# Kernel tuning notes

Hardware: AMD Instinct MI355X
Metric: run time of the kernel (lower is better)

## Reference

```python
import jax, jax.numpy as jnp
import numpy as np

RES_IN, RES_OUT, STRIDE = 14, 7, 2
H1, KD1, AR1 = 4, 32, 2    # per-layer attention blocks
H2, KD2, AR2 = 8, 32, 4    # subsample attention block
DEPTHS = 4


def _bias_idxs(res):
    pts = [(i, j) for i in range(res) for j in range(res)]
    offs, idx = {}, []
    for p1 in pts:
        for p2 in pts:
            o = (abs(p1[0] - p2[0]), abs(p1[1] - p2[1]))
            if o not in offs:
                offs[o] = len(offs)
            idx.append(offs[o])
    return np.array(idx, np.int32).reshape(len(pts), len(pts)), len(offs)


def _bias_idxs_sub(res_in, res_out, stride):
    pts = [(i, j) for i in range(res_in) for j in range(res_in)]
    pts_ = [(i, j) for i in range(res_out) for j in range(res_out)]
    offs, idx = {}, []
    for p1 in pts_:
        for p2 in pts:
            o = (abs(p1[0] * stride - p2[0]), abs(p1[1] * stride - p2[1]))
            if o not in offs:
                offs[o] = len(offs)
            idx.append(offs[o])
    return np.array(idx, np.int32).reshape(len(pts_), len(pts)), len(offs)

IDX1, NOFF1 = _bias_idxs(RES_IN)                     # [196,196], 196 offsets
IDX2, NOFF2 = _bias_idxs_sub(RES_IN, RES_OUT, STRIDE)  # [49,196], 196 offsets


def hardswish(x):
    return x * jnp.clip(x + 3.0, 0.0, 6.0) * (1.0 / 6.0)


def setup_inputs() -> dict:
    key = jax.random.key(0)
    ks = iter(jax.random.split(key, 64))

    def nrm(shape, scale=1.0):
        return jax.random.normal(next(ks), shape, jnp.float32) * scale

    def lin(shape):  # fan-in scaled linear weight, last dim = in_features
        return nrm(shape, (1.0 / shape[-1]) ** 0.5)

    def bn(shape):  # folded BN (scale, shift)
        return 1.0 + nrm(shape, 0.05), nrm(shape, 0.05)

    B, S, C = 256, RES_IN * RES_IN, 256
    d = {"x": nrm((B, S, C))}
    d["attn_Wqkv"] = lin((DEPTHS, 512, 256))
    d["attn_qkv_s"], d["attn_qkv_t"] = bn((DEPTHS, 512))
    d["attn_Wproj"] = lin((DEPTHS, 256, 256))
    d["attn_proj_s"], d["attn_proj_t"] = bn((DEPTHS, 256))
    d["attn_bias"] = nrm((DEPTHS, H1, NOFF1), 0.02)
    d["mlp_W1"] = lin((DEPTHS, 512, 256))
    d["mlp1_s"], d["mlp1_t"] = bn((DEPTHS, 512))
    d["mlp_W2"] = lin((DEPTHS, 256, 512))
    d["mlp2_s"], d["mlp2_t"] = bn((DEPTHS, 256))
    d["sub_Wkv"] = lin((1280, 256))
    d["sub_kv_s"], d["sub_kv_t"] = bn((1280,))
    d["sub_Wq"] = lin((256, 256))
    d["sub_q_s"], d["sub_q_t"] = bn((256,))
    d["sub_Wproj"] = lin((384, 1024))
    d["sub_proj_s"], d["sub_proj_t"] = bn((384,))
    d["sub_bias"] = nrm((H2, NOFF2), 0.02)
    d["smlp_W1"] = lin((768, 384))
    d["smlp1_s"], d["smlp1_t"] = bn((768,))
    d["smlp_W2"] = lin((384, 768))
    d["smlp2_s"], d["smlp2_t"] = bn((384,))
    return d


def reference(x, attn_Wqkv, attn_qkv_s, attn_qkv_t, attn_Wproj, attn_proj_s,
              attn_proj_t, attn_bias, mlp_W1, mlp1_s, mlp1_t, mlp_W2, mlp2_s,
              mlp2_t, sub_Wkv, sub_kv_s, sub_kv_t, sub_Wq, sub_q_s, sub_q_t,
              sub_Wproj, sub_proj_s, sub_proj_t, sub_bias, smlp_W1, smlp1_s,
              smlp1_t, smlp_W2, smlp2_s, smlp2_t):
    B, S, C = x.shape
    idx1 = jnp.asarray(IDX1)
    idx2 = jnp.asarray(IDX2)
    scale1 = KD1 ** -0.5
    scale2 = KD2 ** -0.5

    # DEPTHS x (residual attention + residual MLP), eval-mode BN folded to scale/shift
    for l in range(DEPTHS):
        qkv = (x @ attn_Wqkv[l].T) * attn_qkv_s[l] + attn_qkv_t[l]      # [B,S,512]
        qkv = qkv.reshape(B, S, H1, 2 * KD1 + AR1 * KD1)
        q, k, v = qkv[..., :KD1], qkv[..., KD1:2 * KD1], qkv[..., 2 * KD1:]
        logits = jnp.einsum('bqhd,bkhd->bhqk', q, k) * scale1 + attn_bias[l][:, idx1]
        a = jax.nn.softmax(logits, axis=-1)
        o = jnp.einsum('bhqk,bkhd->bqhd', a, v).reshape(B, S, H1 * AR1 * KD1)
        x = x + ((hardswish(o) @ attn_Wproj[l].T) * attn_proj_s[l] + attn_proj_t[l])
        h = hardswish((x @ mlp_W1[l].T) * mlp1_s[l] + mlp1_t[l])
        x = x + ((h @ mlp_W2[l].T) * mlp2_s[l] + mlp2_t[l])

    # attention subsample block (no residual on attention path)
    kv = ((x @ sub_Wkv.T) * sub_kv_s + sub_kv_t).reshape(B, S, H2, KD2 + AR2 * KD2)
    k, v = kv[..., :KD2], kv[..., KD2:]
    xq = x.reshape(B, RES_IN, RES_IN, C)[:, ::STRIDE, ::STRIDE].reshape(B, RES_OUT * RES_OUT, C)
    q = ((xq @ sub_Wq.T) * sub_q_s + sub_q_t).reshape(B, RES_OUT * RES_OUT, H2, KD2)
    logits = jnp.einsum('bqhd,bkhd->bhqk', q, k) * scale2 + sub_bias[:, idx2]
    a = jax.nn.softmax(logits, axis=-1)
    o = jnp.einsum('bhqk,bkhd->bqhd', a, v).reshape(B, RES_OUT * RES_OUT, H2 * AR2 * KD2)
    x = (hardswish(o) @ sub_Wproj.T) * sub_proj_s + sub_proj_t            # [B,49,384]

    # residual MLP after subsample
    h = hardswish((x @ smlp_W1.T) * smlp1_s + smlp1_t)
    x = x + ((h @ smlp_W2.T) * smlp2_s + smlp2_t)
    return x
```

## Files before the change

kernel.cpp:

```cpp
#include <hip/hip_runtime.h>

typedef __attribute__((ext_vector_type(8))) short s16x8;
typedef __attribute__((ext_vector_type(4))) short s16x4;
typedef __attribute__((ext_vector_type(4))) float f32x4;
typedef __attribute__((ext_vector_type(8))) __fp16 f16x8;
typedef __attribute__((ext_vector_type(2))) __fp16 f16x2;

#define AS1 __attribute__((address_space(1)))
#define AS3 __attribute__((address_space(3)))

__device__ __forceinline__ short h16(float f) {
  __fp16 t = (__fp16)f;
  return *(short*)&t;
}
__device__ __forceinline__ float h2f(short s) {
  __fp16 t = *(__fp16*)&s;
  return (float)t;
}
__device__ __forceinline__ unsigned pkh2(float a, float b) {
  f16x2 h = __builtin_amdgcn_cvt_pkrtz(a, b);
  return *(unsigned*)&h;
}
__device__ __forceinline__ float hswish(float v) { return v * fminf(fmaxf(v + 3.f, 0.f), 6.f) * (1.f / 6.f); }
__device__ __forceinline__ int iabs(int v) { return v < 0 ? -v : v; }
__device__ __forceinline__ int gmap(int r) {
  int bb = r / 49, p = r - bb * 49;
  int i = p / 7, j = p - i * 7;
  return bb * 196 + i * 28 + j * 2;
}

template <int ACT, int RES, int WF, int WH, int GATHER>
__global__ __launch_bounds__(256) void gemm_k(
    const short* __restrict__ A, const short* __restrict__ W,
    const float* __restrict__ sc, const float* __restrict__ tc,
    const short* __restrict__ Rs, float* __restrict__ oF, short* __restrict__ oH,
    int M, int N, int K, int nwg) {
  __shared__ __align__(16) short As[128 * 64];
  __shared__ __align__(16) short Bs[128 * 64];
  const int tid = threadIdx.x;
  const int lane = tid & 63;
  const int wave = tid >> 6;
  const int wm = wave >> 1, wn = wave & 1;
  const int r15 = lane & 15, kq = lane >> 4;

  const int qc = nwg >> 3, rc = nwg & 7;
  const int xcd = blockIdx.x & 7, off = blockIdx.x >> 3;
  const int wg = (xcd < rc) ? xcd * (qc + 1) + off : rc * (qc + 1) + (xcd - rc) * qc + off;
  const int NTt = N >> 7;
  const int nt = wg % NTt, mt = wg / NTt;
  const int m0 = mt << 7, n0 = nt << 7;

  const int tr = tid >> 3;
  const int col8 = (tid & 7) ^ (tr & 7);
  const short* pa = A + (size_t)(m0 + tr) * K + 8 * col8;
  const short* pb = W + (size_t)(n0 + tr) * K + 8 * col8;
  short* la = As + tid * 8;
  short* lb = Bs + tid * 8;

  f32x4 acc[4][4] = {};
  const int NT = K >> 6;

#define ISSUE(kt)                                                                     \
  {                                                                                   \
    _Pragma("unroll") for (int i = 0; i < 4; ++i) {                                   \
      const short* ga;                                                                \
      if (GATHER)                                                                     \
        ga = A + (size_t)gmap(m0 + tr + 32 * i) * K + 8 * col8 + (kt) * 64;           \
      else                                                                            \
        ga = pa + (size_t)(32 * i) * K + (kt) * 64;                                   \
      __builtin_amdgcn_global_load_lds((const AS1 void*)ga,                           \
                                       (AS3 void*)(la + i * 2048), 16, 0, 0);         \
      __builtin_amdgcn_global_load_lds(                                               \
          (const AS1 void*)(pb + (size_t)(32 * i) * K + (kt) * 64),                   \
          (AS3 void*)(lb + i * 2048), 16, 0, 0);                                      \
    }                                                                                 \
  }

  ISSUE(0)
  for (int kt = 0; kt < NT; ++kt) {
    __syncthreads();
    f16x8 af[2][4], bq[2][4];
#pragma unroll
    for (int s = 0; s < 2; ++s) {
      const int cb = s * 64 + kq * 16;
#pragma unroll
      for (int f = 0; f < 4; ++f) {
        int rowA = wm * 64 + f * 16 + r15;
        af[s][f] = *(const f16x8*)((const char*)As + ((rowA * 128 + cb) ^ ((rowA & 7) << 4)));
        int rowB = wn * 64 + f * 16 + r15;
        bq[s][f] = *(const f16x8*)((const char*)Bs + ((rowB * 128 + cb) ^ ((rowB & 7) << 4)));
      }
    }
    __syncthreads();
    if (kt + 1 < NT) ISSUE(kt + 1)
    __builtin_amdgcn_sched_barrier(0);
#pragma unroll
    for (int s = 0; s < 2; ++s)
#pragma unroll
      for (int fm = 0; fm < 4; ++fm)
#pragma unroll
        for (int fn = 0; fn < 4; ++fn)
          acc[fm][fn] = __builtin_amdgcn_mfma_f32_16x16x32_f16(af[s][fm], bq[s][fn], acc[fm][fn], 0, 0, 0);
  }
#undef ISSUE

#pragma unroll
  for (int fn = 0; fn < 4; ++fn) {
    const int cn = n0 + wn * 64 + fn * 16 + r15;
    const float scl = sc[cn], tcl = tc[cn];
#pragma unroll
    for (int fm = 0; fm < 4; ++fm) {
#pragma unroll
      for (int j = 0; j < 4; ++j) {
        const int rm = m0 + wm * 64 + fm * 16 + kq * 4 + j;
        float v = acc[fm][fn][j] * scl + tcl;
        if (ACT) v = hswish(v);
        size_t off2 = (size_t)rm * N + cn;
        if (RES) v += h2f(Rs[off2]);
        if (WF) oF[off2] = v;
        if (WH) oH[off2] = h16(v);
      }
    }
  }
}

__global__ __launch_bounds__(256) void attn_mfma_k(const short* __restrict__ QKV,
                                                   const float* __restrict__ BT,
                                                   short* __restrict__ O) {
  __shared__ __align__(16) short Vt[64 * 232];
  __shared__ __align__(16) short P[4 * 16 * 232];
  const int b = blockIdx.x >> 2, h = blockIdx.x & 3;
  const int tid = threadIdx.x;
  const int lane = tid & 63, wave = tid >> 6;
  const int l15 = lane & 15, g = lane >> 4, g4 = g * 4;
  const short* base = QKV + (size_t)b * (196 * 512);

  for (int c = tid; c < 1152; c += 256) {
    int v = c / 18, u = c - v * 18;
    *((unsigned*)Vt + v * 116 + 98 + u) = 0;
  }
  for (int c = tid; c < 768; c += 256) {
    int r = c / 12, u = c - r * 12;
    *((unsigned*)P + r * 116 + 104 + u) = 0;
  }
  for (int c = tid; c < 3136; c += 256) {
    int vp8 = c & 7, rest = c >> 3;
    int vg = rest / 98, kp = rest - vg * 98;
    int vp = vg * 8 + vp8;
    const short* s = base + (size_t)(2 * kp) * 512 + h * 128 + 64 + 2 * vp;
    unsigned a0 = *(const unsigned*)s;
    unsigned a1 = *(const unsigned*)(s + 512);
    *((unsigned*)Vt + (2 * vp) * 116 + kp) = __builtin_amdgcn_perm(a1, a0, 0x05040100u);
    *((unsigned*)Vt + (2 * vp + 1) * 116 + kp) = __builtin_amdgcn_perm(a1, a0, 0x07060302u);
  }
  __syncthreads();

  f16x8 kf[13];
  {
    const short* kb = base + h * 128 + 32 + 8 * g;
#pragma unroll
    for (int t = 0; t < 13; ++t) {
      int kr = 16 * t + l15;
      if (kr > 195) kr = 195;
      kf[t] = *(const f16x8*)(kb + (size_t)kr * 512);
    }
  }

  for (int qt = wave; qt < 13; qt += 4) {
    int qr = 16 * qt + l15;
    if (qr > 195) qr = 195;
    f16x8 qf = *(const f16x8*)(base + (size_t)qr * 512 + h * 128 + 8 * g);
    f32x4 s[13];
    __builtin_amdgcn_s_setprio(1);
#pragma unroll
    for (int t = 0; t < 13; ++t)
      s[t] = __builtin_amdgcn_mfma_f32_16x16x32_f16(kf[t], qf, f32x4{0.f, 0.f, 0.f, 0.f}, 0, 0, 0);
    __builtin_amdgcn_s_setprio(0);

    const float* bt = BT + ((size_t)(h * 208 + 16 * qt + l15)) * 224 + 4 * g;
    float m = -1e30f;
#pragma unroll
    for (int t = 0; t < 13; ++t) {
      f32x4 bv = *(const f32x4*)(bt + 16 * t);
#pragma unroll
      for (int j = 0; j < 4; ++j) {
        float v = fmaf(s[t][j], 0.17677669529663687f, bv[j]);
        s[t][j] = v;
        m = fmaxf(m, v);
      }
    }
    m = fmaxf(m, __shfl_xor(m, 16));
    m = fmaxf(m, __shfl_xor(m, 32));
    float sum = 0.f;
#pragma unroll
    for (int t = 0; t < 13; ++t)
#pragma unroll
      for (int j = 0; j < 4; ++j) {
        float p = __expf(s[t][j] - m);
        s[t][j] = p;
        sum += p;
      }
    sum += __shfl_xor(sum, 16);
    sum += __shfl_xor(sum, 32);
    const float inv = 1.f / sum;
    unsigned* pw = (unsigned*)P + wave * (16 * 116) + l15 * 116;
#pragma unroll
    for (int t = 0; t < 13; ++t) {
      pw[8 * t + 2 * g] = pkh2(s[t][0] * inv, s[t][1] * inv);
      pw[8 * t + 2 * g + 1] = pkh2(s[t][2] * inv, s[t][3] * inv);
    }
    asm volatile("s_waitcnt lgkmcnt(0)" ::: "memory");
    __builtin_amdgcn_sched_barrier(0);

    f32x4 o[4] = {};
    const short* pr = P + wave * (16 * 232) + l15 * 232 + 8 * g;
    const short* vr = Vt + l15 * 232 + 8 * g;
    __builtin_amdgcn_s_setprio(1);
#pragma unroll
    for (int kb = 0; kb < 7; ++kb) {
      f16x8 pa = *(const f16x8*)(pr + 32 * kb);
#pragma unroll
      for (int vt = 0; vt < 4; ++vt) {
        f16x8 vb = *(const f16x8*)(vr + vt * 16 * 232 + 32 * kb);
        o[vt] = __builtin_amdgcn_mfma_f32_16x16x32_f16(pa, vb, o[vt], 0, 0, 0);
      }
    }
    __builtin_amdgcn_s_setprio(0);
#pragma unroll
    for (int vt = 0; vt < 4; ++vt)
#pragma unroll
      for (int j = 0; j < 4; ++j) {
        int qo = 16 * qt + g4 + j;
        if (qo < 196)
          O[(size_t)(b * 196 + qo) * 256 + h * 64 + vt * 16 + l15] = h16(hswish(o[vt][j]));
      }
  }
}

__global__ __launch_bounds__(256) void subattn_mfma_k(const short* __restrict__ KVg,
                                                      const short* __restrict__ Qg,
                                                      const float* __restrict__ BT,
                                                      short* __restrict__ O2) {
  __shared__ __align__(16) short Vt[64 * 232];
  __shared__ __align__(16) short P[4 * 16 * 232];
  const int b = blockIdx.x >> 3, h = blockIdx.x & 7;
  const int tid = threadIdx.x;
  const int lane = tid & 63, wave = tid >> 6;
  const int l15 = lane & 15, g = lane >> 4, g4 = g * 4;
  const short* base = KVg + (size_t)b * (196 * 1280) + h * 160;

  for (int c = tid; c < 1152; c += 256) {
    int v = c / 18, u = c - v * 18;
    *((unsigned*)Vt + v * 116 + 98 + u) = 0;
  }
  for (int c = tid; c < 768; c += 256) {
    int r = c / 12, u = c - r * 12;
    *((unsigned*)P + r * 116 + 104 + u) = 0;
  }

  f16x8 kf[13];
#pragma unroll
  for (int t = 0; t < 13; ++t) {
    int kr = 16 * t + l15;
    if (kr > 195) kr = 195;
    kf[t] = *(const f16x8*)(base + (size_t)kr * 1280 + 8 * g);
  }

  f32x4 s[13];
  float inv;
  const int qt = wave;

  for (int half = 0; half < 2; ++half) {
    if (half) __syncthreads();
    for (int c = tid; c < 3136; c += 256) {
      int vp8 = c & 7, rest = c >> 3;
      int vg = rest / 98, kp = rest - vg * 98;
      int vp = vg * 8 + vp8;
      const short* sp = base + (size_t)(2 * kp) * 1280 + 32 + 64 * half + 2 * vp;
      unsigned a0 = *(const unsigned*)sp;
      unsigned a1 = *(const unsigned*)(sp + 1280);
      *((unsigned*)Vt + (2 * vp) * 116 + kp) = __builtin_amdgcn_perm(a1, a0, 0x05040100u);
      *((unsigned*)Vt + (2 * vp + 1) * 116 + kp) = __builtin_amdgcn_perm(a1, a0, 0x07060302u);
    }
    __syncthreads();

    if (half == 0) {
      int qr = 16 * qt + l15;
      int qc = qr > 48 ? 48 : qr;
      f16x8 qf = *(const f16x8*)(Qg + (size_t)(b * 49 + qc) * 256 + h * 32 + 8 * g);
      __builtin_amdgcn_s_setprio(1);
#pragma unroll
      for (int t = 0; t < 13; ++t)
        s[t] = __builtin_amdgcn_mfma_f32_16x16x32_f16(kf[t], qf, f32x4{0.f, 0.f, 0.f, 0.f}, 0, 0, 0);
      __builtin_amdgcn_s_setprio(0);
      const float* bt = BT + ((size_t)(h * 64 + qr)) * 224 + 4 * g;
      float m = -1e30f;
#pragma unroll
      for (int t = 0; t < 13; ++t) {
        f32x4 bv = *(const f32x4*)(bt + 16 * t);
#pragma unroll
        for (int j = 0; j < 4; ++j) {
          float v = fmaf(s[t][j], 0.17677669529663687f, bv[j]);
          s[t][j] = v;
          m = fmaxf(m, v);
        }
      }
      m = fmaxf(m, __shfl_xor(m, 16));
      m = fmaxf(m, __shfl_xor(m, 32));
      float sum = 0.f;
#pragma unroll
      for (int t = 0; t < 13; ++t)
#pragma unroll
        for (int j = 0; j < 4; ++j) {
          float p = __expf(s[t][j] - m);
          s[t][j] = p;
          sum += p;
        }
      sum += __shfl_xor(sum, 16);
      sum += __shfl_xor(sum, 32);
      inv = 1.f / sum;
      unsigned* pw = (unsigned*)P + wave * (16 * 116) + l15 * 116;
#pragma unroll
      for (int t = 0; t < 13; ++t) {
        pw[8 * t + 2 * g] = pkh2(s[t][0] * inv, s[t][1] * inv);
        pw[8 * t + 2 * g + 1] = pkh2(s[t][2] * inv, s[t][3] * inv);
      }
      asm volatile("s_waitcnt lgkmcnt(0)" ::: "memory");
      __builtin_amdgcn_sched_barrier(0);
    }

    f32x4 o[4] = {};
    const short* pr = P + wave * (16 * 232) + l15 * 232 + 8 * g;
    const short* vr = Vt + l15 * 232 + 8 * g;
    __builtin_amdgcn_s_setprio(1);
#pragma unroll
    for (int kb = 0; kb < 7; ++kb) {
      f16x8 pa = *(const f16x8*)(pr + 32 * kb);
#pragma unroll
      for (int vt = 0; vt < 4; ++vt) {
        f16x8 vb = *(const f16x8*)(vr + vt * 16 * 232 + 32 * kb);
        o[vt] = __builtin_amdgcn_mfma_f32_16x16x32_f16(pa, vb, o[vt], 0, 0, 0);
      }
    }
    __builtin_amdgcn_s_setprio(0);
#pragma unroll
    for (int vt = 0; vt < 4; ++vt)
#pragma unroll
      for (int j = 0; j < 4; ++j) {
        int qo = 16 * qt + g4 + j;
        if (qo < 49)
          O2[(size_t)(b * 49 + qo) * 1024 + h * 128 + half * 64 + vt * 16 + l15] =
              h16(hswish(o[vt][j]));
      }
  }
}

struct Cast9 {
  const float* s[9];
  unsigned off[10];
};
__global__ void cast9_k(Cast9 c, short* __restrict__ WH) {
  int i4 = blockIdx.x * 256 + threadIdx.x;
  int e0 = i4 * 4;
  if (e0 >= 3211264) return;
  int seg = 0;
#pragma unroll
  for (int k = 1; k < 9; ++k) seg += (e0 >= (int)c.off[k]);
  const float4 v = *(const float4*)(c.s[seg] + (e0 - c.off[seg]));
  s16x4 r;
  r[0] = h16(v.x); r[1] = h16(v.y); r[2] = h16(v.z); r[3] = h16(v.w);
  *(s16x4*)(WH + e0) = r;
}

__global__ void cast_h(const float* __restrict__ s, short* __restrict__ d, int n4) {
  int i = blockIdx.x * 256 + threadIdx.x;
  if (i >= n4) return;
  const float4 v = ((const float4*)s)[i];
  s16x4 r;
  r[0] = h16(v.x); r[1] = h16(v.y); r[2] = h16(v.z); r[3] = h16(v.w);
  ((s16x4*)d)[i] = r;
}

__global__ void btab1_k(const float* __restrict__ ab, float* __restrict__ T) {
  int i = blockIdx.x * 256 + threadIdx.x;
  if (i >= 745472) return;
  int k = i % 224;
  int rest = i / 224;
  int q = rest % 208;
  int lh = rest / 208;
  float v = -30000.f;
  if (k < 196) {
    int qc = q < 196 ? q : 195;
    int qi = qc / 14, qj = qc - 14 * qi, ki = k / 14, kj = k - 14 * ki;
    v = ab[lh * 196 + iabs(qi - ki) * 14 + iabs(qj - kj)];
  }
  T[i] = v;
}

__global__ void btab2_k(const float* __restrict__ sb, float* __restrict__ T) {
  int i = blockIdx.x * 256 + threadIdx.x;
  if (i >= 114688) return;
  int k = i % 224;
  int rest = i / 224;
  int q = rest % 64;
  int h = rest / 64;
  float v = -30000.f;
  if (k < 196) {
    int qc = q < 49 ? q : 48;
    int qi = qc / 7, qj = qc - 7 * qi, ki = k / 14, kj = k - 14 * ki;
    v = sb[h * 196 + iabs(2 * qi - ki) * 14 + iabs(2 * qj - kj)];
  }
  T[i] = v;
}

extern "C" void kernel_launch(void* const* d_in, const int* in_sizes, int n_in,
                              void* d_out, int out_size, void* d_ws, size_t ws_size,
                              hipStream_t stream) {
  (void)in_sizes; (void)n_in; (void)out_size; (void)ws_size;
  const float* x = (const float*)d_in[0];
  const float* Wqkv = (const float*)d_in[1];
  const float* qkvs = (const float*)d_in[2];
  const float* qkvt = (const float*)d_in[3];
  const float* Wproj = (const float*)d_in[4];
  const float* projs = (const float*)d_in[5];
  const float* projt = (const float*)d_in[6];
  const float* abias = (const float*)d_in[7];
  const float* W1 = (const float*)d_in[8];
  const float* m1s = (const float*)d_in[9];
  const float* m1t = (const float*)d_in[10];
  const float* W2 = (const float*)d_in[11];
  const float* m2s = (const float*)d_in[12];
  const float* m2t = (const float*)d_in[13];
  const float* Wkv = (const float*)d_in[14];
  const float* kvs = (const float*)d_in[15];
  const float* kvt = (const float*)d_in[16];
  const float* Wq = (const float*)d_in[17];
  const float* qss = (const float*)d_in[18];
  const float* qst = (const float*)d_in[19];
  const float* Wp2 = (const float*)d_in[20];
  const float* p2s = (const float*)d_in[21];
  const float* p2t = (const float*)d_in[22];
  const float* sbias = (const float*)d_in[23];
  const float* Ws1 = (const float*)d_in[24];
  const float* s1s = (const float*)d_in[25];
  const float* s1t = (const float*)d_in[26];
  const float* Ws2 = (const float*)d_in[27];
  const float* s2s = (const float*)d_in[28];
  const float* s2t = (const float*)d_in[29];

  char* ws = (char*)d_ws;
  short* WH = (short*)ws;
  short* WHqkv = WH;
  short* WHproj = WH + 524288;
  short* WH1 = WH + 786432;
  short* WH2 = WH + 1310720;
  short* WHkv = WH + 1835008;
  short* WHq = WH + 2162688;
  short* WHp2 = WH + 2228224;
  short* WHs1 = WH + 2621440;
  short* WHs2 = WH + 2916352;

  float* T1 = (float*)(ws + 6422528);
  float* T2 = (float*)(ws + 9404416);
  short* Xh = (short*)(ws + 9863168);
  short* QKVh = (short*)(ws + 35553280);
  short* Hh = QKVh;
  short* Oh = (short*)(ws + 86933504);
  short* KVh = (short*)(ws + 35553280);
  short* Qh = (short*)(ws + 170426368);
  short* O2h = (short*)(ws + 9863168);
  short* X2h = (short*)(ws + 35553280);
  short* H2h = (short*)(ws + 45187072);

  Cast9 c9;
  c9.s[0] = Wqkv; c9.s[1] = Wproj; c9.s[2] = W1; c9.s[3] = W2; c9.s[4] = Wkv;
  c9.s[5] = Wq; c9.s[6] = Wp2; c9.s[7] = Ws1; c9.s[8] = Ws2;
  c9.off[0] = 0; c9.off[1] = 524288; c9.off[2] = 786432; c9.off[3] = 1310720;
  c9.off[4] = 1835008; c9.off[5] = 2162688; c9.off[6] = 2228224;
  c9.off[7] = 2621440; c9.off[8] = 2916352; c9.off[9] = 3211264;
  cast9_k<<<3136, 256, 0, stream>>>(c9, WH);
  btab1_k<<<2912, 256, 0, stream>>>(abias, T1);
  btab2_k<<<448, 256, 0, stream>>>(sbias, T2);
  cast_h<<<12544, 256, 0, stream>>>(x, Xh, 3211264);

  for (int l = 0; l < 4; ++l) {
    gemm_k<0, 0, 0, 1, 0><<<392 * 4, 256, 0, stream>>>(
        Xh, WHqkv + l * 131072, qkvs + l * 512, qkvt + l * 512,
        nullptr, nullptr, QKVh, 50176, 512, 256, 392 * 4);
    attn_mfma_k<<<1024, 256, 0, stream>>>(QKVh, T1 + l * 186368, Oh);
    gemm_k<0, 1, 0, 1, 0><<<392 * 2, 256, 0, stream>>>(
        Oh, WHproj + l * 65536, projs + l * 256, projt + l * 256,
        Xh, nullptr, Xh, 50176, 256, 256, 392 * 2);
    gemm_k<1, 0, 0, 1, 0><<<392 * 4, 256, 0, stream>>>(
        Xh, WH1 + l * 131072, m1s + l * 512, m1t + l * 512,
        nullptr, nullptr, Hh, 50176, 512, 256, 392 * 4);
    gemm_k<0, 1, 0, 1, 0><<<392 * 2, 256, 0, stream>>>(
        Hh, WH2 + l * 131072, m2s + l * 256, m2t + l * 256,
        Xh, nullptr, Xh, 50176, 256, 512, 392 * 2);
  }
  gemm_k<0, 0, 0, 1, 0><<<392 * 10, 256, 0, stream>>>(
      Xh, WHkv, kvs, kvt, nullptr, nullptr, KVh, 50176, 1280, 256, 392 * 10);
  gemm_k<0, 0, 0, 1, 1><<<98 * 2, 256, 0, stream>>>(
      Xh, WHq, qss, qst, nullptr, nullptr, Qh, 12544, 256, 256, 98 * 2);
  subattn_mfma_k<<<2048, 256, 0, stream>>>(KVh, Qh, T2, O2h);
  gemm_k<0, 0, 0, 1, 0><<<98 * 3, 256, 0, stream>>>(
      O2h, WHp2, p2s, p2t, nullptr, nullptr, X2h, 12544, 384, 1024, 98 * 3);
  gemm_k<1, 0, 0, 1, 0><<<98 * 6, 256, 0, stream>>>(
      X2h, WHs1, s1s, s1t, nullptr, nullptr, H2h, 12544, 768, 384, 98 * 6);
  gemm_k<0, 1, 1, 0, 0><<<98 * 3, 256, 0, stream>>>(
      H2h, WHs2, s2s, s2t, X2h, (float*)d_out, nullptr, 12544, 384, 768, 98 * 3);
}
```

Before: 748.4 us.

## Shrink attention LDS footprint, use 16x16x16 PV MFMA, exp2 softmax, preload Q

```diff
diff --git a/kernel.cpp b/kernel.cpp
--- a/kernel.cpp
+++ b/kernel.cpp
@@ -4,6 +4,7 @@
 typedef __attribute__((ext_vector_type(4))) short s16x4;
 typedef __attribute__((ext_vector_type(4))) float f32x4;
 typedef __attribute__((ext_vector_type(8))) __fp16 f16x8;
+typedef __attribute__((ext_vector_type(4))) __fp16 f16x4;
 typedef __attribute__((ext_vector_type(2))) __fp16 f16x2;
 
 #define AS1 __attribute__((address_space(1)))
@@ -28,6 +29,8 @@
   int i = p / 7, j = p - i * 7;
   return bb * 196 + i * 28 + j * 2;
 }
+
+#define SC2 0.25503509f
 
 template <int ACT, int RES, int WF, int WH, int GATHER>
 __global__ __launch_bounds__(256) void gemm_k(
@@ -124,24 +127,30 @@
   }
 }
 
-__global__ __launch_bounds__(256) void attn_mfma_k(const short* __restrict__ QKV,
-                                                   const float* __restrict__ BT,
-                                                   short* __restrict__ O) {
-  __shared__ __align__(16) short Vt[64 * 232];
-  __shared__ __align__(16) short P[4 * 16 * 232];
+__global__ __launch_bounds__(256, 3) void attn_mfma_k(const short* __restrict__ QKV,
+                                                      const float* __restrict__ BT,
+                                                      short* __restrict__ O) {
+  __shared__ __align__(16) short Vt[64 * 212];
+  __shared__ __align__(16) short P[64 * 212];
   const int b = blockIdx.x >> 2, h = blockIdx.x & 3;
   const int tid = threadIdx.x;
   const int lane = tid & 63, wave = tid >> 6;
   const int l15 = lane & 15, g = lane >> 4, g4 = g * 4;
   const short* base = QKV + (size_t)b * (196 * 512);
 
-  for (int c = tid; c < 1152; c += 256) {
-    int v = c / 18, u = c - v * 18;
-    *((unsigned*)Vt + v * 116 + 98 + u) = 0;
-  }
-  for (int c = tid; c < 768; c += 256) {
-    int r = c / 12, u = c - r * 12;
-    *((unsigned*)P + r * 116 + 104 + u) = 0;
+  f16x8 kf[13];
+  {
+    const short* kb = base + h * 128 + 32 + 8 * g;
+#pragma unroll
+    for (int t = 0; t < 13; ++t) {
+      int kr = 16 * t + l15;
+      if (kr > 195) kr = 195;
+      kf[t] = *(const f16x8*)(kb + (size_t)kr * 512);
+    }
+  }
+  for (int c = tid; c < 512; c += 256) {
+    int v = c >> 3, u = c & 7;
+    *((unsigned*)Vt + v * 106 + 98 + u) = 0;
   }
   for (int c = tid; c < 3136; c += 256) {
     int vp8 = c & 7, rest = c >> 3;
@@ -150,31 +159,28 @@
     const short* s = base + (size_t)(2 * kp) * 512 + h * 128 + 64 + 2 * vp;
     unsigned a0 = *(const unsigned*)s;
     unsigned a1 = *(const unsigned*)(s + 512);
-    *((unsigned*)Vt + (2 * vp) * 116 + kp) = __builtin_amdgcn_perm(a1, a0, 0x05040100u);
-    *((unsigned*)Vt + (2 * vp + 1) * 116 + kp) = __builtin_amdgcn_perm(a1, a0, 0x07060302u);
+    *((unsigned*)Vt + (2 * vp) * 106 + kp) = __builtin_amdgcn_perm(a1, a0, 0x05040100u);
+    *((unsigned*)Vt + (2 * vp + 1) * 106 + kp) = __builtin_amdgcn_perm(a1, a0, 0x07060302u);
   }
   __syncthreads();
 
-  f16x8 kf[13];
-  {
-    const short* kb = base + h * 128 + 32 + 8 * g;
-#pragma unroll
-    for (int t = 0; t < 13; ++t) {
-      int kr = 16 * t + l15;
-      if (kr > 195) kr = 195;
-      kf[t] = *(const f16x8*)(kb + (size_t)kr * 512);
-    }
-  }
-
-  for (int qt = wave; qt < 13; qt += 4) {
-    int qr = 16 * qt + l15;
+  f16x8 qf4[4];
+#pragma unroll
+  for (int i = 0; i < 4; ++i) {
+    int qr = 16 * (wave + 4 * i) + l15;
     if (qr > 195) qr = 195;
-    f16x8 qf = *(const f16x8*)(base + (size_t)qr * 512 + h * 128 + 8 * g);
+    qf4[i] = *(const f16x8*)(base + (size_t)qr * 512 + h * 128 + 8 * g);
+  }
+
+#pragma unroll
+  for (int i = 0; i < 4; ++i) {
+    const int qt = wave + 4 * i;
+    if (qt >= 13) break;
     f32x4 s[13];
     __builtin_amdgcn_s_setprio(1);
 #pragma unroll
     for (int t = 0; t < 13; ++t)
-      s[t] = __builtin_amdgcn_mfma_f32_16x16x32_f16(kf[t], qf, f32x4{0.f, 0.f, 0.f, 0.f}, 0, 0, 0);
+      s[t] = __builtin_amdgcn_mfma_f32_16x16x32_f16(kf[t], qf4[i], f32x4{0.f, 0.f, 0.f, 0.f}, 0, 0, 0);
     __builtin_amdgcn_s_setprio(0);
 
     const float* bt = BT + ((size_t)(h * 208 + 16 * qt + l15)) * 224 + 4 * g;
@@ -184,7 +190,7 @@
       f32x4 bv = *(const f32x4*)(bt + 16 * t);
 #pragma unroll
       for (int j = 0; j < 4; ++j) {
-        float v = fmaf(s[t][j], 0.17677669529663687f, bv[j]);
+        float v = fmaf(s[t][j], SC2, bv[j]);
         s[t][j] = v;
         m = fmaxf(m, v);
       }
@@ -196,33 +202,35 @@
     for (int t = 0; t < 13; ++t)
 #pragma unroll
       for (int j = 0; j < 4; ++j) {
-        float p = __expf(s[t][j] - m);
+        float p = exp2f(s[t][j] - m);
         s[t][j] = p;
         sum += p;
       }
     sum += __shfl_xor(sum, 16);
     sum += __shfl_xor(sum, 32);
     const float inv = 1.f / sum;
-    unsigned* pw = (unsigned*)P + wave * (16 * 116) + l15 * 116;
+    unsigned* pw = (unsigned*)P + (wave * 16 + l15) * 106;
 #pragma unroll
     for (int t = 0; t < 13; ++t) {
-      pw[8 * t + 2 * g] = pkh2(s[t][0] * inv, s[t][1] * inv);
-      pw[8 * t + 2 * g + 1] = pkh2(s[t][2] * inv, s[t][3] * inv);
+      uint2 pk;
+      pk.x = pkh2(s[t][0] * inv, s[t][1] * inv);
+      pk.y = pkh2(s[t][2] * inv, s[t][3] * inv);
+      *(uint2*)(pw + 8 * t + 2 * g) = pk;
     }
     asm volatile("s_waitcnt lgkmcnt(0)" ::: "memory");
     __builtin_amdgcn_sched_barrier(0);
 
     f32x4 o[4] = {};
-    const short* pr = P + wave * (16 * 232) + l15 * 232 + 8 * g;
-    const short* vr = Vt + l15 * 232 + 8 * g;
+    const short* pr = P + (wave * 16 + l15) * 212 + 4 * g;
+    const short* vr = Vt + l15 * 212 + 4 * g;
     __builtin_amdgcn_s_setprio(1);
 #pragma unroll
-    for (int kb = 0; kb < 7; ++kb) {
-      f16x8 pa = *(const f16x8*)(pr + 32 * kb);
+    for (int t = 0; t < 13; ++t) {
+      f16x4 pa = *(const f16x4*)(pr + 16 * t);
 #pragma unroll
       for (int vt = 0; vt < 4; ++vt) {
-        f16x8 vb = *(const f16x8*)(vr + vt * 16 * 232 + 32 * kb);
-        o[vt] = __builtin_amdgcn_mfma_f32_16x16x32_f16(pa, vb, o[vt], 0, 0, 0);
+        f16x4 vb = *(const f16x4*)(vr + vt * 16 * 212 + 16 * t);
+        o[vt] = __builtin_amdgcn_mfma_f32_16x16x16f16(pa, vb, o[vt], 0, 0, 0);
       }
     }
     __builtin_amdgcn_s_setprio(0);
@@ -237,27 +245,18 @@
   }
 }
 
-__global__ __launch_bounds__(256) void subattn_mfma_k(const short* __restrict__ KVg,
-                                                      const short* __restrict__ Qg,
-                                                      const float* __restrict__ BT,
-                                                      short* __restrict__ O2) {
-  __shared__ __align__(16) short Vt[64 * 232];
-  __shared__ __align__(16) short P[4 * 16 * 232];
+__global__ __launch_bounds__(256, 3) void subattn_mfma_k(const short* __restrict__ KVg,
+                                                         const short* __restrict__ Qg,
+                                                         const float* __restrict__ BT,
+                                                         short* __restrict__ O2) {
+  __shared__ __align__(16) short Vt[64 * 212];
+  __shared__ __align__(16) short P[64 * 212];
   const int b = blockIdx.x >> 3, h = blockIdx.x & 7;
   const int tid = threadIdx.x;
   const int lane = tid & 63, wave = tid >> 6;
   const int l15 = lane & 15, g = lane >> 4, g4 = g * 4;
   const short* base = KVg + (size_t)b * (196 * 1280) + h * 160;
 
-  for (int c = tid; c < 1152; c += 256) {
-    int v = c / 18, u = c - v * 18;
-    *((unsigned*)Vt + v * 116 + 98 + u) = 0;
-  }
-  for (int c = tid; c < 768; c += 256) {
-    int r = c / 12, u = c - r * 12;
-    *((unsigned*)P + r * 116 + 104 + u) = 0;
-  }
-
   f16x8 kf[13];
 #pragma unroll
   for (int t = 0; t < 13; ++t) {
@@ -265,10 +264,14 @@
     if (kr > 195) kr = 195;
     kf[t] = *(const f16x8*)(base + (size_t)kr * 1280 + 8 * g);
   }
-
-  f32x4 s[13];
-  float inv;
-  const int qt = wave;
+  int qr = 16 * wave + l15;
+  int qcl = qr > 48 ? 48 : qr;
+  f16x8 qf = *(const f16x8*)(Qg + (size_t)(b * 49 + qcl) * 256 + h * 32 + 8 * g);
+
+  for (int c = tid; c < 512; c += 256) {
+    int v = c >> 3, u = c & 7;
+    *((unsigned*)Vt + v * 106 + 98 + u) = 0;
+  }
 
   for (int half = 0; half < 2; ++half) {
     if (half) __syncthreads();
@@ -279,15 +282,13 @@
       const short* sp = base + (size_t)(2 * kp) * 1280 + 32 + 64 * half + 2 * vp;
       unsigned a0 = *(const unsigned*)sp;
       unsigned a1 = *(const unsigned*)(sp + 1280);
-      *((unsigned*)Vt + (2 * vp) * 116 + kp) = __builtin_amdgcn_perm(a1, a0, 0x05040100u);
-      *((unsigned*)Vt + (2 * vp + 1) * 116 + kp) = __builtin_amdgcn_perm(a1, a0, 0x07060302u);
+      *((unsigned*)Vt + (2 * vp) * 106 + kp) = __builtin_amdgcn_perm(a1, a0, 0x05040100u);
+      *((unsigned*)Vt + (2 * vp + 1) * 106 + kp) = __builtin_amdgcn_perm(a1, a0, 0x07060302u);
     }
     __syncthreads();
 
     if (half == 0) {
-      int qr = 16 * qt + l15;
-      int qc = qr > 48 ? 48 : qr;
-      f16x8 qf = *(const f16x8*)(Qg + (size_t)(b * 49 + qc) * 256 + h * 32 + 8 * g);
+      f32x4 s[13];
       __builtin_amdgcn_s_setprio(1);
 #pragma unroll
       for (int t = 0; t < 13; ++t)
@@ -300,7 +301,7 @@
         f32x4 bv = *(const f32x4*)(bt + 16 * t);
 #pragma unroll
         for (int j = 0; j < 4; ++j) {
-          float v = fmaf(s[t][j], 0.17677669529663687f, bv[j]);
+          float v = fmaf(s[t][j], SC2, bv[j]);
           s[t][j] = v;
           m = fmaxf(m, v);
         }
@@ -312,34 +313,36 @@
       for (int t = 0; t < 13; ++t)
 #pragma unroll
         for (int j = 0; j < 4; ++j) {
-          float p = __expf(s[t][j] - m);
+          float p = exp2f(s[t][j] - m);
           s[t][j] = p;
           sum += p;
         }
       sum += __shfl_xor(sum, 16);
       sum += __shfl_xor(sum, 32);
-      inv = 1.f / sum;
-      unsigned* pw = (unsigned*)P + wave * (16 * 116) + l15 * 116;
+      const float inv = 1.f / sum;
+      unsigned* pw = (unsigned*)P + (wave * 16 + l15) * 106;
 #pragma unroll
       for (int t = 0; t < 13; ++t) {
-        pw[8 * t + 2 * g] = pkh2(s[t][0] * inv, s[t][1] * inv);
-        pw[8 * t + 2 * g + 1] = pkh2(s[t][2] * inv, s[t][3] * inv);
+        uint2 pk;
+        pk.x = pkh2(s[t][0] * inv, s[t][1] * inv);
+        pk.y = pkh2(s[t][2] * inv, s[t][3] * inv);
+        *(uint2*)(pw + 8 * t + 2 * g) = pk;
       }
       asm volatile("s_waitcnt lgkmcnt(0)" ::: "memory");
       __builtin_amdgcn_sched_barrier(0);
     }
 
     f32x4 o[4] = {};
-    const short* pr = P + wave * (16 * 232) + l15 * 232 + 8 * g;
-    const short* vr = Vt + l15 * 232 + 8 * g;
+    const short* pr = P + (wave * 16 + l15) * 212 + 4 * g;
+    const short* vr = Vt + l15 * 212 + 4 * g;
     __builtin_amdgcn_s_setprio(1);
 #pragma unroll
-    for (int kb = 0; kb < 7; ++kb) {
-      f16x8 pa = *(const f16x8*)(pr + 32 * kb);
+    for (int t = 0; t < 13; ++t) {
+      f16x4 pa = *(const f16x4*)(pr + 16 * t);
 #pragma unroll
       for (int vt = 0; vt < 4; ++vt) {
-        f16x8 vb = *(const f16x8*)(vr + vt * 16 * 232 + 32 * kb);
-        o[vt] = __builtin_amdgcn_mfma_f32_16x16x32_f16(pa, vb, o[vt], 0, 0, 0);
+        f16x4 vb = *(const f16x4*)(vr + vt * 16 * 212 + 16 * t);
+        o[vt] = __builtin_amdgcn_mfma_f32_16x16x16f16(pa, vb, o[vt], 0, 0, 0);
       }
     }
     __builtin_amdgcn_s_setprio(0);
@@ -347,7 +350,7 @@
     for (int vt = 0; vt < 4; ++vt)
 #pragma unroll
       for (int j = 0; j < 4; ++j) {
-        int qo = 16 * qt + g4 + j;
+        int qo = 16 * wave + g4 + j;
         if (qo < 49)
           O2[(size_t)(b * 49 + qo) * 1024 + h * 128 + half * 64 + vt * 16 + l15] =
               h16(hswish(o[vt][j]));
@@ -392,7 +395,7 @@
   if (k < 196) {
     int qc = q < 196 ? q : 195;
     int qi = qc / 14, qj = qc - 14 * qi, ki = k / 14, kj = k - 14 * ki;
-    v = ab[lh * 196 + iabs(qi - ki) * 14 + iabs(qj - kj)];
+    v = ab[lh * 196 + iabs(qi - ki) * 14 + iabs(qj - kj)] * 1.4426950408889634f;
   }
   T[i] = v;
 }
@@ -408,7 +411,7 @@
   if (k < 196) {
     int qc = q < 49 ? q : 48;
     int qi = qc / 7, qj = qc - 7 * qi, ki = k / 14, kj = k - 14 * ki;
-    v = sb[h * 196 + iabs(2 * qi - ki) * 14 + iabs(2 * qj - kj)];
+    v = sb[h * 196 + iabs(2 * qi - ki) * 14 + iabs(2 * qj - kj)] * 1.4426950408889634f;
   }
   T[i] = v;
 }
```

Result: slower. 785.2 us (+4.9%).

## Software-pipeline attention q-tiles and prefetch V halves; fold log2e into softmax

Applied to the files above, without the earlier changes.

```diff
diff --git a/kernel.cpp b/kernel.cpp
--- a/kernel.cpp
+++ b/kernel.cpp
@@ -28,6 +28,8 @@
   int i = p / 7, j = p - i * 7;
   return bb * 196 + i * 28 + j * 2;
 }
+
+#define SC2 0.25503509f
 
 template <int ACT, int RES, int WF, int WH, int GATHER>
 __global__ __launch_bounds__(256) void gemm_k(
@@ -135,6 +137,24 @@
   const int l15 = lane & 15, g = lane >> 4, g4 = g * 4;
   const short* base = QKV + (size_t)b * (196 * 512);
 
+  f16x8 kf[13];
+  {
+    const short* kb = base + h * 128 + 32 + 8 * g;
+#pragma unroll
+    for (int t = 0; t < 13; ++t) {
+      int kr = 16 * t + l15;
+      if (kr > 195) kr = 195;
+      kf[t] = *(const f16x8*)(kb + (size_t)kr * 512);
+    }
+  }
+  f16x8 qf4[4];
+#pragma unroll
+  for (int i = 0; i < 4; ++i) {
+    int qr = 16 * (wave + 4 * i) + l15;
+    if (qr > 195) qr = 195;
+    qf4[i] = *(const f16x8*)(base + (size_t)qr * 512 + h * 128 + 8 * g);
+  }
+
   for (int c = tid; c < 1152; c += 256) {
     int v = c / 18, u = c - v * 18;
     *((unsigned*)Vt + v * 116 + 98 + u) = 0;
@@ -147,73 +167,72 @@
     int vp8 = c & 7, rest = c >> 3;
     int vg = rest / 98, kp = rest - vg * 98;
     int vp = vg * 8 + vp8;
-    const short* s = base + (size_t)(2 * kp) * 512 + h * 128 + 64 + 2 * vp;
-    unsigned a0 = *(const unsigned*)s;
-    unsigned a1 = *(const unsigned*)(s + 512);
+    const short* sV = base + (size_t)(2 * kp) * 512 + h * 128 + 64 + 2 * vp;
+    unsigned a0 = *(const unsigned*)sV;
+    unsigned a1 = *(const unsigned*)(sV + 512);
     *((unsigned*)Vt + (2 * vp) * 116 + kp) = __builtin_amdgcn_perm(a1, a0, 0x05040100u);
     *((unsigned*)Vt + (2 * vp + 1) * 116 + kp) = __builtin_amdgcn_perm(a1, a0, 0x07060302u);
   }
   __syncthreads();
 
-  f16x8 kf[13];
-  {
-    const short* kb = base + h * 128 + 32 + 8 * g;
-#pragma unroll
-    for (int t = 0; t < 13; ++t) {
-      int kr = 16 * t + l15;
-      if (kr > 195) kr = 195;
-      kf[t] = *(const f16x8*)(kb + (size_t)kr * 512);
-    }
-  }
-
-  for (int qt = wave; qt < 13; qt += 4) {
-    int qr = 16 * qt + l15;
-    if (qr > 195) qr = 195;
-    f16x8 qf = *(const f16x8*)(base + (size_t)qr * 512 + h * 128 + 8 * g);
-    f32x4 s[13];
-    __builtin_amdgcn_s_setprio(1);
-#pragma unroll
-    for (int t = 0; t < 13; ++t)
-      s[t] = __builtin_amdgcn_mfma_f32_16x16x32_f16(kf[t], qf, f32x4{0.f, 0.f, 0.f, 0.f}, 0, 0, 0);
-    __builtin_amdgcn_s_setprio(0);
-
-    const float* bt = BT + ((size_t)(h * 208 + 16 * qt + l15)) * 224 + 4 * g;
-    float m = -1e30f;
-#pragma unroll
-    for (int t = 0; t < 13; ++t) {
-      f32x4 bv = *(const f32x4*)(bt + 16 * t);
-#pragma unroll
-      for (int j = 0; j < 4; ++j) {
-        float v = fmaf(s[t][j], 0.17677669529663687f, bv[j]);
-        s[t][j] = v;
-        m = fmaxf(m, v);
-      }
-    }
-    m = fmaxf(m, __shfl_xor(m, 16));
-    m = fmaxf(m, __shfl_xor(m, 32));
-    float sum = 0.f;
-#pragma unroll
-    for (int t = 0; t < 13; ++t)
-#pragma unroll
-      for (int j = 0; j < 4; ++j) {
-        float p = __expf(s[t][j] - m);
-        s[t][j] = p;
-        sum += p;
-      }
-    sum += __shfl_xor(sum, 16);
-    sum += __shfl_xor(sum, 32);
-    const float inv = 1.f / sum;
-    unsigned* pw = (unsigned*)P + wave * (16 * 116) + l15 * 116;
-#pragma unroll
-    for (int t = 0; t < 13; ++t) {
-      pw[8 * t + 2 * g] = pkh2(s[t][0] * inv, s[t][1] * inv);
-      pw[8 * t + 2 * g + 1] = pkh2(s[t][2] * inv, s[t][3] * inv);
-    }
-    asm volatile("s_waitcnt lgkmcnt(0)" ::: "memory");
-    __builtin_amdgcn_sched_barrier(0);
-
+  f32x4 s[13];
+#define QK_(ii)                                                                        \
+  {                                                                                    \
+    __builtin_amdgcn_s_setprio(1);                                                     \
+    _Pragma("unroll") for (int t = 0; t < 13; ++t) s[t] =                              \
+        __builtin_amdgcn_mfma_f32_16x16x32_f16(kf[t], qf4[ii],                         \
+                                               f32x4{0.f, 0.f, 0.f, 0.f}, 0, 0, 0);    \
+    __builtin_amdgcn_s_setprio(0);                                                     \
+  }
+#define SM_(qt_)                                                                       \
+  {                                                                                    \
+    const float* bt = BT + ((size_t)(h * 208 + 16 * (qt_) + l15)) * 224 + 4 * g;       \
+    float m = -1e30f;                                                                  \
+    _Pragma("unroll") for (int t = 0; t < 13; ++t) {                                   \
+      f32x4 bv = *(const f32x4*)(bt + 16 * t);                                         \
+      _Pragma("unroll") for (int j = 0; j < 4; ++j) {                                  \
+        float v = fmaf(s[t][j], SC2, bv[j]);                                           \
+        s[t][j] = v;                                                                   \
+        m = fmaxf(m, v);                                                               \
+      }                                                                                \
+    }                                                                                  \
+    m = fmaxf(m, __shfl_xor(m, 16));                                                   \
+    m = fmaxf(m, __shfl_xor(m, 32));                                                   \
+    float sum = 0.f;                                                                   \
+    _Pragma("unroll") for (int t = 0; t < 13; ++t) {                                   \
+      _Pragma("unroll") for (int j = 0; j < 4; ++j) {                                  \
+        float p = exp2f(s[t][j] - m);                                                  \
+        s[t][j] = p;                                                                   \
+        sum += p;                                                                      \
+      }                                                                                \
+    }                                                                                  \
+    sum += __shfl_xor(sum, 16);                                                        \
+    sum += __shfl_xor(sum, 32);                                                        \
+    float inv = 1.f / sum;                                                             \
+    _Pragma("unroll") for (int t = 0; t < 13; ++t) {                                   \
+      s[t][0] *= inv; s[t][1] *= inv; s[t][2] *= inv; s[t][3] *= inv;                  \
+    }                                                                                  \
+  }
+#define PW_()                                                                          \
+  {                                                                                    \
+    unsigned* pw = (unsigned*)P + wave * (16 * 116) + l15 * 116;                       \
+    _Pragma("unroll") for (int t = 0; t < 13; ++t) {                                   \
+      pw[8 * t + 2 * g] = pkh2(s[t][0], s[t][1]);                                      \
+      pw[8 * t + 2 * g + 1] = pkh2(s[t][2], s[t][3]);                                  \
+    }                                                                                  \
+    asm volatile("s_waitcnt lgkmcnt(0)" ::: "memory");                                 \
+    __builtin_amdgcn_sched_barrier(0);                                                 \
+  }
+
+  const int nq = wave ? 3 : 4;
+  QK_(0) SM_(wave) PW_()
+#pragma unroll
+  for (int i = 0; i < 4; ++i) {
+    if (i >= nq) break;
+    const int qt = wave + 4 * i;
+    if (i + 1 < nq) { QK_(i + 1) SM_(wave + 4 * (i + 1)) }
     f32x4 o[4] = {};
-    const short* pr = P + wave * (16 * 232) + l15 * 232 + 8 * g;
+    const short* pr = P + (wave * 16 + l15) * 232 + 8 * g;
     const short* vr = Vt + l15 * 232 + 8 * g;
     __builtin_amdgcn_s_setprio(1);
 #pragma unroll
@@ -234,7 +253,11 @@
         if (qo < 196)
           O[(size_t)(b * 196 + qo) * 256 + h * 64 + vt * 16 + l15] = h16(hswish(o[vt][j]));
       }
-  }
+    if (i + 1 < nq) PW_()
+  }
+#undef QK_
+#undef SM_
+#undef PW_
 }
 
 __global__ __launch_bounds__(256) void subattn_mfma_k(const short* __restrict__ KVg,
@@ -249,15 +272,6 @@
   const int l15 = lane & 15, g = lane >> 4, g4 = g * 4;
   const short* base = KVg + (size_t)b * (196 * 1280) + h * 160;
 
-  for (int c = tid; c < 1152; c += 256) {
-    int v = c / 18, u = c - v * 18;
-    *((unsigned*)Vt + v * 116 + 98 + u) = 0;
-  }
-  for (int c = tid; c < 768; c += 256) {
-    int r = c / 12, u = c - r * 12;
-    *((unsigned*)P + r * 116 + 104 + u) = 0;
-  }
-
   f16x8 kf[13];
 #pragma unroll
   for (int t = 0; t < 13; ++t) {
@@ -265,73 +279,105 @@
     if (kr > 195) kr = 195;
     kf[t] = *(const f16x8*)(base + (size_t)kr * 1280 + 8 * g);
   }
+  const int qr = 16 * wave + l15;
+  const int qcl = qr > 48 ? 48 : qr;
+  f16x8 qf = *(const f16x8*)(Qg + (size_t)(b * 49 + qcl) * 256 + h * 32 + 8 * g);
+
+  for (int c = tid; c < 1152; c += 256) {
+    int v = c / 18, u = c - v * 18;
+    *((unsigned*)Vt + v * 116 + 98 + u) = 0;
+  }
+  for (int c = tid; c < 768; c += 256) {
+    int r = c / 12, u = c - r * 12;
+    *((unsigned*)P + r * 116 + 104 + u) = 0;
+  }
+  for (int c = tid; c < 3136; c += 256) {
+    int vp8 = c & 7, rest = c >> 3;
+    int vg = rest / 98, kp = rest - vg * 98;
+    int vp = vg * 8 + vp8;
+    const short* sp = base + (size_t)(2 * kp) * 1280 + 32 + 2 * vp;
+    unsigned a0 = *(const unsigned*)sp;
+    unsigned a1 = *(const unsigned*)(sp + 1280);
+    *((unsigned*)Vt + (2 * vp) * 116 + kp) = __builtin_amdgcn_perm(a1, a0, 0x05040100u);
+    *((unsigned*)Vt + (2 * vp + 1) * 116 + kp) = __builtin_amdgcn_perm(a1, a0, 0x07060302u);
+  }
+  __syncthreads();
 
   f32x4 s[13];
-  float inv;
-  const int qt = wave;
-
+  __builtin_amdgcn_s_setprio(1);
+#pragma unroll
+  for (int t = 0; t < 13; ++t)
+    s[t] = __builtin_amdgcn_mfma_f32_16x16x32_f16(kf[t], qf, f32x4{0.f, 0.f, 0.f, 0.f}, 0, 0, 0);
+  __builtin_amdgcn_s_setprio(0);
+  {
+    const float* bt = BT + ((size_t)(h * 64 + qr)) * 224 + 4 * g;
+    float m = -1e30f;
+#pragma unroll
+    for (int t = 0; t < 13; ++t) {
+      f32x4 bv = *(const f32x4*)(bt + 16 * t);
+#pragma unroll
+      for (int j = 0; j < 4; ++j) {
+        float v = fmaf(s[t][j], SC2, bv[j]);
+        s[t][j] = v;
+        m = fmaxf(m, v);
+      }
+    }
+    m = fmaxf(m, __shfl_xor(m, 16));
+    m = fmaxf(m, __shfl_xor(m, 32));
+    float sum = 0.f;
+#pragma unroll
+    for (int t = 0; t < 13; ++t)
+#pragma unroll
+      for (int j = 0; j < 4; ++j) {
+        float p = exp2f(s[t][j] - m);
+        s[t][j] = p;
+        sum += p;
+      }
+    sum += __shfl_xor(sum, 16);
+    sum += __shfl_xor(sum, 32);
+    const float inv = 1.f / sum;
+    unsigned* pw = (unsigned*)P + wave * (16 * 116) + l15 * 116;
+#pragma unroll
+    for (int t = 0; t < 13; ++t) {
+      pw[8 * t + 2 * g] = pkh2(s[t][0] * inv, s[t][1] * inv);
+      pw[8 * t + 2 * g + 1] = pkh2(s[t][2] * inv, s[t][3] * inv);
+    }
+    asm volatile("s_waitcnt lgkmcnt(0)" ::: "memory");
+    __builtin_amdgcn_sched_barrier(0);
+  }
+
+  uint2 ra[13];
+#pragma unroll
+  for (int it = 0; it < 13; ++it) {
+    int c = tid + 256 * it;
+    int cc = c < 3136 ? c : 3135;
+    int vp8 = cc & 7, rest = cc >> 3;
+    int vg = rest / 98, kp = rest - vg * 98;
+    int vp = vg * 8 + vp8;
+    const short* sp = base + (size_t)(2 * kp) * 1280 + 32 + 64 + 2 * vp;
+    ra[it].x = *(const unsigned*)sp;
+    ra[it].y = *(const unsigned*)(sp + 1280);
+  }
+
+  const short* pr = P + (wave * 16 + l15) * 232 + 8 * g;
+  const short* vr = Vt + l15 * 232 + 8 * g;
+#pragma unroll
   for (int half = 0; half < 2; ++half) {
-    if (half) __syncthreads();
-    for (int c = tid; c < 3136; c += 256) {
-      int vp8 = c & 7, rest = c >> 3;
-      int vg = rest / 98, kp = rest - vg * 98;
-      int vp = vg * 8 + vp8;
-      const short* sp = base + (size_t)(2 * kp) * 1280 + 32 + 64 * half + 2 * vp;
-      unsigned a0 = *(const unsigned*)sp;
-      unsigned a1 = *(const unsigned*)(sp + 1280);
-      *((unsigned*)Vt + (2 * vp) * 116 + kp) = __builtin_amdgcn_perm(a1, a0, 0x05040100u);
-      *((unsigned*)Vt + (2 * vp + 1) * 116 + kp) = __builtin_amdgcn_perm(a1, a0, 0x07060302u);
-    }
-    __syncthreads();
-
-    if (half == 0) {
-      int qr = 16 * qt + l15;
-      int qc = qr > 48 ? 48 : qr;
-      f16x8 qf = *(const f16x8*)(Qg + (size_t)(b * 49 + qc) * 256 + h * 32 + 8 * g);
-      __builtin_amdgcn_s_setprio(1);
-#pragma unroll
-      for (int t = 0; t < 13; ++t)
-        s[t] = __builtin_amdgcn_mfma_f32_16x16x32_f16(kf[t], qf, f32x4{0.f, 0.f, 0.f, 0.f}, 0, 0, 0);
-      __builtin_amdgcn_s_setprio(0);
-      const float* bt = BT + ((size_t)(h * 64 + qr)) * 224 + 4 * g;
-      float m = -1e30f;
-#pragma unroll
-      for (int t = 0; t < 13; ++t) {
-        f32x4 bv = *(const f32x4*)(bt + 16 * t);
-#pragma unroll
-        for (int j = 0; j < 4; ++j) {
-          float v = fmaf(s[t][j], 0.17677669529663687f, bv[j]);
-          s[t][j] = v;
-          m = fmaxf(m, v);
-        }
-      }
-      m = fmaxf(m, __shfl_xor(m, 16));
-      m = fmaxf(m, __shfl_xor(m, 32));
-      float sum = 0.f;
-#pragma unroll
-      for (int t = 0; t < 13; ++t)
-#pragma unroll
-        for (int j = 0; j < 4; ++j) {
-          float p = __expf(s[t][j] - m);
-          s[t][j] = p;
-          sum += p;
-        }
-      sum += __shfl_xor(sum, 16);
-      sum += __shfl_xor(sum, 32);
-      inv = 1.f / sum;
-      unsigned* pw = (unsigned*)P + wave * (16 * 116) + l15 * 116;
-#pragma unroll
-      for (int t = 0; t < 13; ++t) {
-        pw[8 * t + 2 * g] = pkh2(s[t][0] * inv, s[t][1] * inv);
-        pw[8 * t + 2 * g + 1] = pkh2(s[t][2] * inv, s[t][3] * inv);
-      }
-      asm volatile("s_waitcnt lgkmcnt(0)" ::: "memory");
-      __builtin_amdgcn_sched_barrier(0);
-    }
-
+    if (half) {
+      __syncthreads();
+#pragma unroll
+      for (int it = 0; it < 13; ++it) {
+        int c = tid + 256 * it;
+        if (c >= 3136) break;
+        int vp8 = c & 7, rest = c >> 3;
+        int vg = rest / 98, kp = rest - vg * 98;
+        int vp = vg * 8 + vp8;
+        *((unsigned*)Vt + (2 * vp) * 116 + kp) = __builtin_amdgcn_perm(ra[it].y, ra[it].x, 0x05040100u);
+        *((unsigned*)Vt + (2 * vp + 1) * 116 + kp) = __builtin_amdgcn_perm(ra[it].y, ra[it].x, 0x07060302u);
+      }
+      __syncthreads();
+    }
     f32x4 o[4] = {};
-    const short* pr = P + wave * (16 * 232) + l15 * 232 + 8 * g;
-    const short* vr = Vt + l15 * 232 + 8 * g;
     __builtin_amdgcn_s_setprio(1);
 #pragma unroll
     for (int kb = 0; kb < 7; ++kb) {
@@ -347,7 +393,7 @@
     for (int vt = 0; vt < 4; ++vt)
 #pragma unroll
       for (int j = 0; j < 4; ++j) {
-        int qo = 16 * qt + g4 + j;
+        int qo = 16 * wave + g4 + j;
         if (qo < 49)
           O2[(size_t)(b * 49 + qo) * 1024 + h * 128 + half * 64 + vt * 16 + l15] =
               h16(hswish(o[vt][j]));
@@ -392,7 +438,7 @@
   if (k < 196) {
     int qc = q < 196 ? q : 195;
     int qi = qc / 14, qj = qc - 14 * qi, ki = k / 14, kj = k - 14 * ki;
-    v = ab[lh * 196 + iabs(qi - ki) * 14 + iabs(qj - kj)];
+    v = ab[lh * 196 + iabs(qi - ki) * 14 + iabs(qj - kj)] * 1.4426950408889634f;
   }
   T[i] = v;
 }
@@ -408,7 +454,7 @@
   if (k < 196) {
     int qc = q < 49 ? q : 48;
     int qi = qc / 7, qj = qc - 7 * qi, ki = k / 14, kj = k - 14 * ki;
-    v = sb[h * 196 + iabs(2 * qi - ki) * 14 + iabs(2 * qj - kj)];
+    v = sb[h * 196 + iabs(2 * qi - ki) * 14 + iabs(2 * qj - kj)] * 1.4426950408889634f;
   }
   T[i] = v;
 }
```

New measurement: 786.3 us. 5.1% more time.
